# Kernel tuning notes

Measured on AMD Instinct MI355X. Metric: run time of the kernel, lower is better.

## Reference

```python
import jax, jax.numpy as jnp
import numpy as np

C, H, W = 3, 2048, 2048
N_BOXES = 256
HEIGHT = 32  # target_height


def _make_boxes():
    # Realistic text-line quads: TL, TR, BR, BL corners.
    rng = np.random.RandomState(0)
    x0 = rng.uniform(0, W - 500, N_BOXES)
    y0 = rng.uniform(0, H - 60, N_BOXES)
    bw = rng.uniform(100, 400, N_BOXES)
    bh = rng.uniform(20, 40, N_BOXES)
    p0 = np.stack([x0, y0], -1)
    p1 = np.stack([x0 + bw, y0], -1)
    p2 = np.stack([x0 + bw, y0 + bh], -1)
    p3 = np.stack([x0, y0 + bh], -1)
    return np.stack([p0, p1, p2, p3], 1).astype(np.float32)  # [N,4,2]


def setup_inputs() -> dict:
    key = jax.random.key(0)
    img = jax.random.normal(key, (C, H, W), dtype=jnp.float32)
    boxes = jnp.asarray(_make_boxes())
    scale = jnp.ones((1,), dtype=jnp.float32)
    return {"img": img, "boxes": boxes, "scale": scale}


def reference(img, boxes, scale):
    height = HEIGHT
    boxes = boxes / scale  # [N,4,2]
    img_c, img_h, img_w = img.shape

    h_dists = jnp.linalg.norm(boxes[:, 2] - boxes[:, 1], axis=1)
    w_dists = jnp.linalg.norm(boxes[:, 1] - boxes[:, 0], axis=1)
    # torch .long() truncates toward zero; values are positive here.
    widths = (height * w_dists / jnp.clip(h_dists, 1e-6)).astype(jnp.int32)
    max_w = int(widths.max()) // 8 * 8 + 8  # concrete (data-dependent shape)

    rows = jnp.arange(height, dtype=jnp.float32) / (height - 1)
    cols = jnp.arange(max_w, dtype=jnp.float32)
    y = rows[None, :, None]        # broadcasts to [N,height,max_w]
    x_idx = cols[None, None, :]
    curr_w = widths.astype(jnp.float32)[:, None, None]
    x = x_idx / jnp.clip(curr_w - 1.0, 1.0)

    def _interp(idx):
        v0 = boxes[:, 0, idx][:, None, None]
        v1 = boxes[:, 1, idx][:, None, None]
        v2 = boxes[:, 2, idx][:, None, None]
        v3 = boxes[:, 3, idx][:, None, None]
        return (1 - x) * (1 - y) * v0 + x * (1 - y) * v1 + x * y * v2 + (1 - x) * y * v3

    res_x = _interp(0)  # [N,height,max_w]
    res_y = _interp(1)
    mask = x_idx < curr_w
    grid_c = jnp.where(mask, res_x / (img_w - 1.0) * 2.0 - 1.0, 2.0)
    grid_r = jnp.where(mask, res_y / (img_h - 1.0) * 2.0 - 1.0, 2.0)

    # grid_sample(mode='nearest', padding_mode='zeros', align_corners=True)
    ix = jnp.round((grid_c + 1.0) * (img_w - 1) * 0.5)
    iy = jnp.round((grid_r + 1.0) * (img_h - 1) * 0.5)
    inb = (ix >= 0) & (ix <= img_w - 1) & (iy >= 0) & (iy <= img_h - 1)
    ixc = jnp.clip(ix, 0, img_w - 1).astype(jnp.int32)
    iyc = jnp.clip(iy, 0, img_h - 1).astype(jnp.int32)
    samp = img[:, iyc, ixc]                    # [C,N,height,max_w]
    out = jnp.where(inb[None], samp, 0.0).transpose(1, 0, 2, 3)  # [N,C,height,max_w]

    widths_out = (widths // 8 * 8 + 8).astype(jnp.int32)
    return out, widths_out
```

## Files before the change

kernel.cpp:

```cpp
#include <hip/hip_runtime.h>

constexpr int kC = 3;
constexpr int kH = 2048;
constexpr int kW = 2048;
constexpr int kNB = 256;
constexpr int kHeight = 32;

typedef float f32x4 __attribute__((ext_vector_type(4)));

__global__ __launch_bounds__(256) void extract_kernel(
    const float* __restrict__ img,
    const float* __restrict__ boxes,
    const float* __restrict__ scale,
    float* __restrict__ out,
    int max_w)
{
#pragma clang fp contract(off)
    const int r = blockIdx.y * 4 + threadIdx.y;
    const int b = blockIdx.z;
    const int c0 = (blockIdx.x * 64 + threadIdx.x) * 4;
    if (c0 >= max_w) return;

    const float s = scale[0];
    const float* bx = boxes + b * 8;
    const float p0x = bx[0] / s, p0y = bx[1] / s;
    const float p1x = bx[2] / s, p1y = bx[3] / s;
    const float p2x = bx[4] / s, p2y = bx[5] / s;
    const float p3x = bx[6] / s, p3y = bx[7] / s;

    const float hdx = p2x - p1x, hdy = p2y - p1y;
    const float h_dist = sqrtf(hdx * hdx + hdy * hdy);
    const float wdx = p1x - p0x, wdy = p1y - p0y;
    const float w_dist = sqrtf(wdx * wdx + wdy * wdy);
    const int width = (int)(32.0f * w_dist / fmaxf(h_dist, 1e-6f));
    const float curr_w = (float)width;

    if (r == 0 && c0 == 0) {
        out[(size_t)kNB * kC * kHeight * max_w + b] = (float)(width / 8 * 8 + 8);
    }

    const size_t ch_stride = (size_t)kHeight * max_w;
    const size_t obase = (((size_t)b * kC) * (size_t)kHeight + (size_t)r) * (size_t)max_w + (size_t)c0;

    f32x4 o0 = {0.f, 0.f, 0.f, 0.f};
    f32x4 o1 = {0.f, 0.f, 0.f, 0.f};
    f32x4 o2 = {0.f, 0.f, 0.f, 0.f};

    if (c0 < width) {
        const float y = (float)r / 31.0f;
        const float omy = 1.0f - y;
        const float xden = fmaxf(curr_w - 1.0f, 1.0f);
#pragma unroll
        for (int j = 0; j < 4; ++j) {
            const float cf = (float)(c0 + j);
            if (cf < curr_w) {
                const float x = cf / xden;
                const float omx = 1.0f - x;
                const float w00 = omx * omy;
                const float w10 = x * omy;
                const float w11 = x * y;
                const float w01 = omx * y;
                const float res_x = w00 * p0x + w10 * p1x + w11 * p2x + w01 * p3x;
                const float res_y = w00 * p0y + w10 * p1y + w11 * p2y + w01 * p3y;

                const float grid_c = res_x / 2047.0f * 2.0f - 1.0f;
                const float grid_r = res_y / 2047.0f * 2.0f - 1.0f;
                const float fix = rintf((grid_c + 1.0f) * 2047.0f * 0.5f);
                const float fiy = rintf((grid_r + 1.0f) * 2047.0f * 0.5f);
                const bool inb = (fix >= 0.0f) && (fix <= 2047.0f) &&
                                 (fiy >= 0.0f) && (fiy <= 2047.0f);
                const int ixc = (int)fminf(fmaxf(fix, 0.0f), 2047.0f);
                const int iyc = (int)fminf(fmaxf(fiy, 0.0f), 2047.0f);

                const size_t ipix = (size_t)iyc * kW + (size_t)ixc;
                const float v0 = img[ipix];
                const float v1 = img[(size_t)kH * kW + ipix];
                const float v2 = img[2 * (size_t)kH * kW + ipix];
                o0[j] = inb ? v0 : 0.0f;
                o1[j] = inb ? v1 : 0.0f;
                o2[j] = inb ? v2 : 0.0f;
            }
        }
    }

    *(f32x4*)(out + obase) = o0;
    *(f32x4*)(out + obase + ch_stride) = o1;
    *(f32x4*)(out + obase + 2 * ch_stride) = o2;
}

extern "C" void kernel_launch(void* const* d_in, const int* in_sizes, int n_in,
                              void* d_out, int out_size, void* d_ws, size_t ws_size,
                              hipStream_t stream) {
    const float* img   = (const float*)d_in[0];
    const float* boxes = (const float*)d_in[1];
    const float* scale = (const float*)d_in[2];
    float* out = (float*)d_out;

    const int max_w = (out_size - kNB) / (kNB * kC * kHeight);
    const int quads = max_w / 4;

    dim3 grid((quads + 63) / 64, kHeight / 4, kNB);
    extract_kernel<<<grid, dim3(64, 4, 1), 0, stream>>>(img, boxes, scale, out, max_w);
}
```

Measured before the change: 24.84 us.

## Precompute per-box parameters in a prep kernel and shrink extract blocks

Adds a small prep kernel that computes the scaled corners, width, reciprocal denominator and output widths once per box into the workspace. The extract kernel then loads these instead of recomputing divisions and square roots in every thread, uses reciprocal multiplies in place of divides, drops the contract(off) pragma, and launches 64-thread blocks with one row per block. The cost is a second kernel launch and a dependency between the two kernels. Reciprocal multiplication and FMA contraction can change rounding, so nearest-pixel indices may differ from the reference at rounding boundaries.

New measurement: 24.76 us. No clear change (-0.3%).

```diff
diff --git a/kernel.cpp b/kernel.cpp
--- a/kernel.cpp
+++ b/kernel.cpp
@@ -8,36 +8,54 @@
 
 typedef float f32x4 __attribute__((ext_vector_type(4)));
 
-__global__ __launch_bounds__(256) void extract_kernel(
-    const float* __restrict__ img,
+__global__ __launch_bounds__(256) void boxprep_kernel(
     const float* __restrict__ boxes,
     const float* __restrict__ scale,
+    float* __restrict__ params,
+    float* __restrict__ out_tail)
+{
+    const int b = threadIdx.x;
+    const float s = scale[0];
+    const float* bx = boxes + b * 8;
+    float p[8];
+#pragma unroll
+    for (int k = 0; k < 8; ++k) p[k] = bx[k] / s;
+
+    const float hdx = p[4] - p[2], hdy = p[5] - p[3];
+    const float h_dist = sqrtf(hdx * hdx + hdy * hdy);
+    const float wdx = p[2] - p[0], wdy = p[3] - p[1];
+    const float w_dist = sqrtf(wdx * wdx + wdy * wdy);
+    const int width = (int)(32.0f * w_dist / fmaxf(h_dist, 1e-6f));
+    const float curr_w = (float)width;
+    const float inv_xden = 1.0f / fmaxf(curr_w - 1.0f, 1.0f);
+
+    float* pp = params + b * 16;
+#pragma unroll
+    for (int k = 0; k < 8; ++k) pp[k] = p[k];
+    pp[8] = curr_w;
+    pp[9] = inv_xden;
+
+    out_tail[b] = (float)(width / 8 * 8 + 8);
+}
+
+__global__ __launch_bounds__(64) void extract_kernel(
+    const float* __restrict__ img,
+    const float* __restrict__ params,
     float* __restrict__ out,
     int max_w)
 {
-#pragma clang fp contract(off)
-    const int r = blockIdx.y * 4 + threadIdx.y;
+    const int r = blockIdx.y;
     const int b = blockIdx.z;
     const int c0 = (blockIdx.x * 64 + threadIdx.x) * 4;
     if (c0 >= max_w) return;
 
-    const float s = scale[0];
-    const float* bx = boxes + b * 8;
-    const float p0x = bx[0] / s, p0y = bx[1] / s;
-    const float p1x = bx[2] / s, p1y = bx[3] / s;
-    const float p2x = bx[4] / s, p2y = bx[5] / s;
-    const float p3x = bx[6] / s, p3y = bx[7] / s;
-
-    const float hdx = p2x - p1x, hdy = p2y - p1y;
-    const float h_dist = sqrtf(hdx * hdx + hdy * hdy);
-    const float wdx = p1x - p0x, wdy = p1y - p0y;
-    const float w_dist = sqrtf(wdx * wdx + wdy * wdy);
-    const int width = (int)(32.0f * w_dist / fmaxf(h_dist, 1e-6f));
-    const float curr_w = (float)width;
-
-    if (r == 0 && c0 == 0) {
-        out[(size_t)kNB * kC * kHeight * max_w + b] = (float)(width / 8 * 8 + 8);
-    }
+    const float* pp = params + b * 16;
+    const float p0x = pp[0], p0y = pp[1];
+    const float p1x = pp[2], p1y = pp[3];
+    const float p2x = pp[4], p2y = pp[5];
+    const float p3x = pp[6], p3y = pp[7];
+    const float curr_w = pp[8];
+    const float inv_xden = pp[9];
 
     const size_t ch_stride = (size_t)kHeight * max_w;
     const size_t obase = (((size_t)b * kC) * (size_t)kHeight + (size_t)r) * (size_t)max_w + (size_t)c0;
@@ -46,15 +64,15 @@
     f32x4 o1 = {0.f, 0.f, 0.f, 0.f};
     f32x4 o2 = {0.f, 0.f, 0.f, 0.f};
 
-    if (c0 < width) {
+    if ((float)c0 < curr_w) {
         const float y = (float)r / 31.0f;
         const float omy = 1.0f - y;
-        const float xden = fmaxf(curr_w - 1.0f, 1.0f);
+        constexpr float invW1 = 1.0f / 2047.0f;
 #pragma unroll
         for (int j = 0; j < 4; ++j) {
             const float cf = (float)(c0 + j);
             if (cf < curr_w) {
-                const float x = cf / xden;
+                const float x = cf * inv_xden;
                 const float omx = 1.0f - x;
                 const float w00 = omx * omy;
                 const float w10 = x * omy;
@@ -63,8 +81,8 @@
                 const float res_x = w00 * p0x + w10 * p1x + w11 * p2x + w01 * p3x;
                 const float res_y = w00 * p0y + w10 * p1y + w11 * p2y + w01 * p3y;
 
-                const float grid_c = res_x / 2047.0f * 2.0f - 1.0f;
-                const float grid_r = res_y / 2047.0f * 2.0f - 1.0f;
+                const float grid_c = res_x * invW1 * 2.0f - 1.0f;
+                const float grid_r = res_y * invW1 * 2.0f - 1.0f;
                 const float fix = rintf((grid_c + 1.0f) * 2047.0f * 0.5f);
                 const float fiy = rintf((grid_r + 1.0f) * 2047.0f * 0.5f);
                 const bool inb = (fix >= 0.0f) && (fix <= 2047.0f) &&
@@ -95,10 +113,14 @@
     const float* boxes = (const float*)d_in[1];
     const float* scale = (const float*)d_in[2];
     float* out = (float*)d_out;
+    float* params = (float*)d_ws;
 
     const int max_w = (out_size - kNB) / (kNB * kC * kHeight);
     const int quads = max_w / 4;
 
-    dim3 grid((quads + 63) / 64, kHeight / 4, kNB);
-    extract_kernel<<<grid, dim3(64, 4, 1), 0, stream>>>(img, boxes, scale, out, max_w);
+    boxprep_kernel<<<1, kNB, 0, stream>>>(boxes, scale, params,
+                                          out + (size_t)kNB * kC * kHeight * max_w);
+
+    dim3 grid((quads + 63) / 64, kHeight, kNB);
+    extract_kernel<<<grid, dim3(64, 1, 1), 0, stream>>>(img, params, out, max_w);
 }
```

## Restructure grid to one block per box-channel-half with swizzled block order

Applied to the files above, without the earlier changes.

Launches a 1D grid of blocks, each handling one box, one channel and half the rows. Threads loop over row/quad pairs and block IDs are swizzled, likely to spread boxes across XCDs. Each thread now gathers one channel instead of three, and several divides become reciprocal multiplies. Dropping the fp contract(off) pragma and using reciprocals can change rounding of computed pixel indices at .5 boundaries relative to the reference.

Result: slower. 29.26 us (+17.8%).

```diff
diff --git a/kernel.cpp b/kernel.cpp
--- a/kernel.cpp
+++ b/kernel.cpp
@@ -13,13 +13,14 @@
     const float* __restrict__ boxes,
     const float* __restrict__ scale,
     float* __restrict__ out,
-    int max_w)
+    int max_w, int nq, float inv_nq)
 {
-#pragma clang fp contract(off)
-    const int r = blockIdx.y * 4 + threadIdx.y;
-    const int b = blockIdx.z;
-    const int c0 = (blockIdx.x * 64 + threadIdx.x) * 4;
-    if (c0 >= max_w) return;
+    const int bid = blockIdx.x;
+    const int swz = (bid & 7) * 192 + (bid >> 3);
+    const int rhalf = swz & 1;
+    const int chb = swz >> 1;
+    const int b = chb / 3;
+    const int ch = chb - b * 3;
 
     const float s = scale[0];
     const float* bx = boxes + b * 8;
@@ -34,58 +35,58 @@
     const float w_dist = sqrtf(wdx * wdx + wdy * wdy);
     const int width = (int)(32.0f * w_dist / fmaxf(h_dist, 1e-6f));
     const float curr_w = (float)width;
+    const float inv_xden = 1.0f / fmaxf(curr_w - 1.0f, 1.0f);
 
-    if (r == 0 && c0 == 0) {
+    if (ch == 0 && rhalf == 0 && threadIdx.x == 0) {
         out[(size_t)kNB * kC * kHeight * max_w + b] = (float)(width / 8 * 8 + 8);
     }
 
-    const size_t ch_stride = (size_t)kHeight * max_w;
-    const size_t obase = (((size_t)b * kC) * (size_t)kHeight + (size_t)r) * (size_t)max_w + (size_t)c0;
+    const float* plane = img + (size_t)ch * (kH * kW);
+    float* dst = out + ((size_t)(b * kC + ch) * kHeight + rhalf * 16) * (size_t)max_w;
 
-    f32x4 o0 = {0.f, 0.f, 0.f, 0.f};
-    f32x4 o1 = {0.f, 0.f, 0.f, 0.f};
-    f32x4 o2 = {0.f, 0.f, 0.f, 0.f};
+    constexpr float invW1 = 1.0f / 2047.0f;
+    const int total = 16 * nq;
 
-    if (c0 < width) {
-        const float y = (float)r / 31.0f;
-        const float omy = 1.0f - y;
-        const float xden = fmaxf(curr_w - 1.0f, 1.0f);
+    for (int idx = threadIdx.x; idx < total; idx += 256) {
+        int r16 = (int)((float)idx * inv_nq);
+        if (r16 * nq > idx) --r16;
+        if ((r16 + 1) * nq <= idx) ++r16;
+        const int qi = idx - r16 * nq;
+        const int c0 = qi * 4;
+        const int r = rhalf * 16 + r16;
+
+        f32x4 o = {0.f, 0.f, 0.f, 0.f};
+
+        if ((float)c0 < curr_w) {
+            const float y = (float)r / 31.0f;
+            const float omy = 1.0f - y;
 #pragma unroll
-        for (int j = 0; j < 4; ++j) {
-            const float cf = (float)(c0 + j);
-            if (cf < curr_w) {
-                const float x = cf / xden;
-                const float omx = 1.0f - x;
-                const float w00 = omx * omy;
-                const float w10 = x * omy;
-                const float w11 = x * y;
-                const float w01 = omx * y;
-                const float res_x = w00 * p0x + w10 * p1x + w11 * p2x + w01 * p3x;
-                const float res_y = w00 * p0y + w10 * p1y + w11 * p2y + w01 * p3y;
-
-                const float grid_c = res_x / 2047.0f * 2.0f - 1.0f;
-                const float grid_r = res_y / 2047.0f * 2.0f - 1.0f;
-                const float fix = rintf((grid_c + 1.0f) * 2047.0f * 0.5f);
-                const float fiy = rintf((grid_r + 1.0f) * 2047.0f * 0.5f);
-                const bool inb = (fix >= 0.0f) && (fix <= 2047.0f) &&
-                                 (fiy >= 0.0f) && (fiy <= 2047.0f);
-                const int ixc = (int)fminf(fmaxf(fix, 0.0f), 2047.0f);
-                const int iyc = (int)fminf(fmaxf(fiy, 0.0f), 2047.0f);
-
-                const size_t ipix = (size_t)iyc * kW + (size_t)ixc;
-                const float v0 = img[ipix];
-                const float v1 = img[(size_t)kH * kW + ipix];
-                const float v2 = img[2 * (size_t)kH * kW + ipix];
-                o0[j] = inb ? v0 : 0.0f;
-                o1[j] = inb ? v1 : 0.0f;
-                o2[j] = inb ? v2 : 0.0f;
+            for (int j = 0; j < 4; ++j) {
+                const float cf = (float)(c0 + j);
+                if (cf < curr_w) {
+                    const float x = cf * inv_xden;
+                    const float omx = 1.0f - x;
+                    const float w00 = omx * omy;
+                    const float w10 = x * omy;
+                    const float w11 = x * y;
+                    const float w01 = omx * y;
+                    const float res_x = ((w00 * p0x + w10 * p1x) + w11 * p2x) + w01 * p3x;
+                    const float res_y = ((w00 * p0y + w10 * p1y) + w11 * p2y) + w01 * p3y;
+                    const float grid_c = res_x * invW1 * 2.0f - 1.0f;
+                    const float grid_r = res_y * invW1 * 2.0f - 1.0f;
+                    const float fix = rintf((grid_c + 1.0f) * 2047.0f * 0.5f);
+                    const float fiy = rintf((grid_r + 1.0f) * 2047.0f * 0.5f);
+                    const bool inb = (fix >= 0.0f) && (fix <= 2047.0f) &&
+                                     (fiy >= 0.0f) && (fiy <= 2047.0f);
+                    const int ixc = (int)fminf(fmaxf(fix, 0.0f), 2047.0f);
+                    const int iyc = (int)fminf(fmaxf(fiy, 0.0f), 2047.0f);
+                    o[j] = inb ? plane[(size_t)iyc * kW + (size_t)ixc] : 0.0f;
+                }
             }
         }
+
+        *(f32x4*)(dst + (size_t)r16 * max_w + c0) = o;
     }
-
-    *(f32x4*)(out + obase) = o0;
-    *(f32x4*)(out + obase + ch_stride) = o1;
-    *(f32x4*)(out + obase + 2 * ch_stride) = o2;
 }
 
 extern "C" void kernel_launch(void* const* d_in, const int* in_sizes, int n_in,
@@ -97,8 +98,10 @@
     float* out = (float*)d_out;
 
     const int max_w = (out_size - kNB) / (kNB * kC * kHeight);
-    const int quads = max_w / 4;
+    const int nq = max_w / 4;
+    const float inv_nq = 1.0f / (float)nq;
 
-    dim3 grid((quads + 63) / 64, kHeight / 4, kNB);
-    extract_kernel<<<grid, dim3(64, 4, 1), 0, stream>>>(img, boxes, scale, out, max_w);
+    const int nblocks = kNB * kC * 2;
+    extract_kernel<<<nblocks, 256, 0, stream>>>(img, boxes, scale, out,
+                                                max_w, nq, inv_nq);
 }
```

## Split padding zero-fill into separate kernel and shrink extract blocks to one row

Applied to the files above, without the earlier changes.

Moves the writing of zero padding beyond each box's width into a dedicated zero-fill kernel, one block per box and channel, which also writes the widths output. The gather kernel now uses 64-thread blocks covering a single row, and whole waves exit early when the column quad lies past the box width. The intent is to avoid launching gather work for mostly padded regions and to get finer-grained scheduling. The cost is a second kernel launch and many tiny blocks, some of which do nothing.

After: 31.28 us. 25.9% more time.

```diff
diff --git a/kernel.cpp b/kernel.cpp
--- a/kernel.cpp
+++ b/kernel.cpp
@@ -8,7 +8,50 @@
 
 typedef float f32x4 __attribute__((ext_vector_type(4)));
 
-__global__ __launch_bounds__(256) void extract_kernel(
+__device__ __forceinline__ int box_width(const float* __restrict__ boxes,
+                                         float s, int b) {
+#pragma clang fp contract(off)
+    const float* bx = boxes + b * 8;
+    const float p0x = bx[0] / s, p0y = bx[1] / s;
+    const float p1x = bx[2] / s, p1y = bx[3] / s;
+    const float p2x = bx[4] / s, p2y = bx[5] / s;
+    const float hdx = p2x - p1x, hdy = p2y - p1y;
+    const float h_dist = sqrtf(hdx * hdx + hdy * hdy);
+    const float wdx = p1x - p0x, wdy = p1y - p0y;
+    const float w_dist = sqrtf(wdx * wdx + wdy * wdy);
+    return (int)(32.0f * w_dist / fmaxf(h_dist, 1e-6f));
+}
+
+__global__ __launch_bounds__(256) void zerofill_kernel(
+    const float* __restrict__ boxes,
+    const float* __restrict__ scale,
+    float* __restrict__ out,
+    int max_w, int nq)
+{
+    const int bc = blockIdx.x;
+    const int b = bc / 3;
+    const int ch = bc - b * 3;
+
+    const float s = scale[0];
+    const int width = box_width(boxes, s, b);
+    const int qstart = (width + 3) >> 2;
+
+    if (ch == 0 && threadIdx.x == 0) {
+        out[(size_t)kNB * kC * kHeight * max_w + b] = (float)(width / 8 * 8 + 8);
+    }
+
+    float* plane = out + (size_t)(b * kC + ch) * kHeight * max_w;
+    const f32x4 z = {0.f, 0.f, 0.f, 0.f};
+#pragma unroll 4
+    for (int r = 0; r < kHeight; ++r) {
+        float* rowp = plane + (size_t)r * max_w;
+        for (int q = qstart + threadIdx.x; q < nq; q += 256) {
+            *(f32x4*)(rowp + q * 4) = z;
+        }
+    }
+}
+
+__global__ __launch_bounds__(64) void extract_kernel(
     const float* __restrict__ img,
     const float* __restrict__ boxes,
     const float* __restrict__ scale,
@@ -16,10 +59,9 @@
     int max_w)
 {
 #pragma clang fp contract(off)
-    const int r = blockIdx.y * 4 + threadIdx.y;
+    const int r = blockIdx.y;
     const int b = blockIdx.z;
     const int c0 = (blockIdx.x * 64 + threadIdx.x) * 4;
-    if (c0 >= max_w) return;
 
     const float s = scale[0];
     const float* bx = boxes + b * 8;
@@ -35,9 +77,7 @@
     const int width = (int)(32.0f * w_dist / fmaxf(h_dist, 1e-6f));
     const float curr_w = (float)width;
 
-    if (r == 0 && c0 == 0) {
-        out[(size_t)kNB * kC * kHeight * max_w + b] = (float)(width / 8 * 8 + 8);
-    }
+    if (c0 >= width) return;
 
     const size_t ch_stride = (size_t)kHeight * max_w;
     const size_t obase = (((size_t)b * kC) * (size_t)kHeight + (size_t)r) * (size_t)max_w + (size_t)c0;
@@ -46,40 +86,38 @@
     f32x4 o1 = {0.f, 0.f, 0.f, 0.f};
     f32x4 o2 = {0.f, 0.f, 0.f, 0.f};
 
-    if (c0 < width) {
-        const float y = (float)r / 31.0f;
-        const float omy = 1.0f - y;
-        const float xden = fmaxf(curr_w - 1.0f, 1.0f);
+    const float y = (float)r / 31.0f;
+    const float omy = 1.0f - y;
+    const float xden = fmaxf(curr_w - 1.0f, 1.0f);
 #pragma unroll
-        for (int j = 0; j < 4; ++j) {
-            const float cf = (float)(c0 + j);
-            if (cf < curr_w) {
-                const float x = cf / xden;
-                const float omx = 1.0f - x;
-                const float w00 = omx * omy;
-                const float w10 = x * omy;
-                const float w11 = x * y;
-                const float w01 = omx * y;
-                const float res_x = w00 * p0x + w10 * p1x + w11 * p2x + w01 * p3x;
-                const float res_y = w00 * p0y + w10 * p1y + w11 * p2y + w01 * p3y;
+    for (int j = 0; j < 4; ++j) {
+        const float cf = (float)(c0 + j);
+        if (cf < curr_w) {
+            const float x = cf / xden;
+            const float omx = 1.0f - x;
+            const float w00 = omx * omy;
+            const float w10 = x * omy;
+            const float w11 = x * y;
+            const float w01 = omx * y;
+            const float res_x = w00 * p0x + w10 * p1x + w11 * p2x + w01 * p3x;
+            const float res_y = w00 * p0y + w10 * p1y + w11 * p2y + w01 * p3y;
 
-                const float grid_c = res_x / 2047.0f * 2.0f - 1.0f;
-                const float grid_r = res_y / 2047.0f * 2.0f - 1.0f;
-                const float fix = rintf((grid_c + 1.0f) * 2047.0f * 0.5f);
-                const float fiy = rintf((grid_r + 1.0f) * 2047.0f * 0.5f);
-                const bool inb = (fix >= 0.0f) && (fix <= 2047.0f) &&
-                                 (fiy >= 0.0f) && (fiy <= 2047.0f);
-                const int ixc = (int)fminf(fmaxf(fix, 0.0f), 2047.0f);
-                const int iyc = (int)fminf(fmaxf(fiy, 0.0f), 2047.0f);
+            const float grid_c = res_x / 2047.0f * 2.0f - 1.0f;
+            const float grid_r = res_y / 2047.0f * 2.0f - 1.0f;
+            const float fix = rintf((grid_c + 1.0f) * 2047.0f * 0.5f);
+            const float fiy = rintf((grid_r + 1.0f) * 2047.0f * 0.5f);
+            const bool inb = (fix >= 0.0f) && (fix <= 2047.0f) &&
+                             (fiy >= 0.0f) && (fiy <= 2047.0f);
+            const int ixc = (int)fminf(fmaxf(fix, 0.0f), 2047.0f);
+            const int iyc = (int)fminf(fmaxf(fiy, 0.0f), 2047.0f);
 
-                const size_t ipix = (size_t)iyc * kW + (size_t)ixc;
-                const float v0 = img[ipix];
-                const float v1 = img[(size_t)kH * kW + ipix];
-                const float v2 = img[2 * (size_t)kH * kW + ipix];
-                o0[j] = inb ? v0 : 0.0f;
-                o1[j] = inb ? v1 : 0.0f;
-                o2[j] = inb ? v2 : 0.0f;
-            }
+            const size_t ipix = (size_t)iyc * kW + (size_t)ixc;
+            const float v0 = img[ipix];
+            const float v1 = img[(size_t)kH * kW + ipix];
+            const float v2 = img[2 * (size_t)kH * kW + ipix];
+            o0[j] = inb ? v0 : 0.0f;
+            o1[j] = inb ? v1 : 0.0f;
+            o2[j] = inb ? v2 : 0.0f;
         }
     }
 
@@ -97,8 +135,10 @@
     float* out = (float*)d_out;
 
     const int max_w = (out_size - kNB) / (kNB * kC * kHeight);
-    const int quads = max_w / 4;
+    const int nq = max_w / 4;
 
-    dim3 grid((quads + 63) / 64, kHeight / 4, kNB);
-    extract_kernel<<<grid, dim3(64, 4, 1), 0, stream>>>(img, boxes, scale, out, max_w);
+    zerofill_kernel<<<kNB * kC, 256, 0, stream>>>(boxes, scale, out, max_w, nq);
+
+    dim3 grid((nq + 63) / 64, kHeight, kNB);
+    extract_kernel<<<grid, dim3(64, 1, 1), 0, stream>>>(img, boxes, scale, out, max_w);
 }
```
